# Optimization experiments

Measured on AMD Instinct MI355X. Metric: run time of the kernel, lower is better.

Reference implementation:

```python
import jax, jax.numpy as jnp
import numpy as np
import math

B, H, S, DK = 4, 16, 2048, 64

def setup_inputs() -> dict:
    key = jax.random.key(0)
    kq, kk, kv, km = jax.random.split(key, 4)
    q = jax.random.normal(kq, (B, H, S, DK), dtype=jnp.float32)
    k = jax.random.normal(kk, (B, H, S, DK), dtype=jnp.float32)
    v = jax.random.normal(kv, (B, H, S, DK), dtype=jnp.float32)
    mask = jax.random.randint(km, (B, 1, 1, S), 0, 2, dtype=jnp.int32)
    return {"q": q, "k": k, "v": v, "mask": mask}

def reference(q, k, v, mask):
    scale = 1.0 / math.sqrt(DK)
    # scores: [B, H, S, S]
    scores = jnp.einsum('bhqd,bhkd->bhqk', q, k) * scale
    scores = jnp.where(mask == 0, jnp.float32(-1e9), scores)
    attn = jax.nn.softmax(scores, axis=-1)
    out = jnp.einsum('bhqk,bhkd->bhqd', attn, v)
    return out
```

## Files before the change

### kernel.cpp

```cpp
#include <hip/hip_runtime.h>
#include <hip/hip_bf16.h>

#define S_LEN 2048
#define D_K   64
#define N_H   16
#define N_B   4
#define KVB   64
#define QPB   128
#define NQB   (S_LEN / QPB)
#define NBH   (N_B * N_H)
#define WS_NEED (2L * NBH * S_LEN * D_K * 2 + 4L * S_LEN * 4 + 16)

typedef __attribute__((ext_vector_type(8)))  short bf16x8;
typedef __attribute__((ext_vector_type(16))) float f32x16;
typedef unsigned int u32;
typedef __attribute__((ext_vector_type(4))) u32 u32x4;

__device__ inline short f2bfs(float x) {
    __hip_bfloat16 h = __float2bfloat16(x);
    return __builtin_bit_cast(short, h);
}

__device__ inline bf16x8 cvt8(const float* __restrict__ p) {
    float4 a = *(const float4*)p;
    float4 b = *(const float4*)(p + 4);
    bf16x8 f;
    f[0] = f2bfs(a.x); f[1] = f2bfs(a.y);
    f[2] = f2bfs(a.z); f[3] = f2bfs(a.w);
    f[4] = f2bfs(b.x); f[5] = f2bfs(b.y);
    f[6] = f2bfs(b.z); f[7] = f2bfs(b.w);
    return f;
}

__device__ inline bf16x8 cvt8s(const float* __restrict__ p, float s) {
    float4 a = *(const float4*)p;
    float4 b = *(const float4*)(p + 4);
    bf16x8 f;
    f[0] = f2bfs(a.x * s); f[1] = f2bfs(a.y * s);
    f[2] = f2bfs(a.z * s); f[3] = f2bfs(a.w * s);
    f[4] = f2bfs(b.x * s); f[5] = f2bfs(b.y * s);
    f[6] = f2bfs(b.z * s); f[7] = f2bfs(b.w * s);
    return f;
}

__device__ inline int vswz(int d) { return ((d & 7) ^ ((d >> 3) & 7)) << 4; }

__device__ inline void gld16(const void* g, void* l) {
    __builtin_amdgcn_global_load_lds(
        (const __attribute__((address_space(1))) void*)g,
        (__attribute__((address_space(3))) void*)l, 16, 0, 0);
}

__global__ __launch_bounds__(64)
void mask_scan(const int* __restrict__ mask, int* __restrict__ idx,
               int* __restrict__ cnt) {
    const int b = blockIdx.x, lane = threadIdx.x;
    const int* mb = mask + b * S_LEN;
    int base = 0;
    for (int j0 = 0; j0 < S_LEN; j0 += 64) {
        int mv = mb[j0 + lane];
        unsigned long long ball = __ballot(mv != 0);
        int pos = base + __popcll(ball & ((1ull << lane) - 1ull));
        if (mv) idx[b * S_LEN + pos] = j0 + lane;
        base += __popcll(ball);
    }
    if (lane == 0) cnt[b] = base;
}

__global__ __launch_bounds__(256)
void gather_cvt(const float* __restrict__ k, const float* __restrict__ v,
                const int* __restrict__ idx, const int* __restrict__ cnt,
                short* __restrict__ kc, short* __restrict__ vt) {
    const int bid = blockIdx.x, bh = bid >> 5, i0 = (bid & 31) * 64;
    const int b = bh >> 4;
    const int m = cnt[b];
    if (i0 >= ((m + 63) & ~63)) return;
    const int t = threadIdx.x;
    const int r = t >> 2, c0 = (t & 3) * 16;
    const int i = i0 + r;

    __shared__ __align__(16) short tile_[64][72];
    bf16x8 fv0, fv1, fk0, fk1;
    if (i < m) {
        const int src = idx[b * S_LEN + i];
        const float* kp = k + ((long)bh * S_LEN + src) * D_K + c0;
        const float* vp = v + ((long)bh * S_LEN + src) * D_K + c0;
        fk0 = cvt8(kp); fk1 = cvt8(kp + 8);
        fv0 = cvt8(vp); fv1 = cvt8(vp + 8);
    } else {
#pragma unroll
        for (int j = 0; j < 8; ++j) { fk0[j] = 0; fk1[j] = 0; fv0[j] = 0; fv1[j] = 0; }
    }
    short* kdst = kc + ((long)bh * S_LEN + i) * D_K + c0;
    *(bf16x8*)kdst       = fk0;
    *(bf16x8*)(kdst + 8) = fk1;
    *(bf16x8*)&tile_[r][c0]     = fv0;
    *(bf16x8*)&tile_[r][c0 + 8] = fv1;
    __syncthreads();
    const int dd = t >> 2, k0 = (t & 3) * 16;
    bf16x8 h0, h1;
#pragma unroll
    for (int j = 0; j < 8; ++j) {
        h0[j] = tile_[k0 + j][dd];
        h1[j] = tile_[k0 + 8 + j][dd];
    }
    short* dst = vt + ((long)bh * D_K + dd) * S_LEN + i0 + k0;
    *(bf16x8*)dst       = h0;
    *(bf16x8*)(dst + 8) = h1;
}

__global__ __launch_bounds__(256)
void attn_fwd(const float* __restrict__ q, const short* __restrict__ kbf,
              const short* __restrict__ vtb, const int* __restrict__ cnt,
              float* __restrict__ out) {
    const int id      = blockIdx.x;
    const int logical = (id & 7) * 128 + (id >> 3);
    const int bh      = logical >> 4;
    const int qblk    = logical & 15;
    const int b       = bh >> 4;
    const int t       = threadIdx.x;
    const int lane    = t & 63;
    const int wq      = t >> 6;
    const int hb      = lane >> 5;
    const int ql      = lane & 31;

    const int m   = cnt[b];
    const int NTr = (m + 63) >> 6;

    __shared__ __align__(16) short kbuf[2][KVB * D_K];
    __shared__ __align__(16) short vbuf[2][D_K * KVB];

    const float scale2 = 0.125f * 1.44269504f;
    const long  baseq  = (long)bh * S_LEN * D_K;
    const int   qrow0  = qblk * QPB + wq * 32;

    bf16x8 qf[4];
    {
        const float* qp = q + baseq + (long)(qrow0 + ql) * D_K + hb * 8;
#pragma unroll
        for (int kd = 0; kd < 4; ++kd) qf[kd] = cvt8s(qp + kd * 16, scale2);
    }

    const int lrow = lane >> 3, lchk = lane & 7;
    const int rA = wq * 16 + lrow;
    const int rB = rA + 8;
    const short* ksA = kbf + baseq + (long)rA * D_K + ((lchk ^ (rA & 7)) * 8);
    const short* ksB = kbf + baseq + (long)rB * D_K + ((lchk ^ (rB & 7)) * 8);
    const short* vsA = vtb + ((long)bh * D_K + rA) * S_LEN + ((lchk ^ ((rA & 7) ^ ((rA >> 3) & 7))) * 8);
    const short* vsB = vtb + ((long)bh * D_K + rB) * S_LEN + ((lchk ^ ((rB & 7) ^ ((rB >> 3) & 7))) * 8);

    auto STAGE_K = [&](int sel) {
        char* kdst = (char*)&kbuf[sel][0];
        gld16(ksA, kdst + (wq * 16) * 128);
        gld16(ksB, kdst + (wq * 16 + 8) * 128);
        ksA += KVB * D_K; ksB += KVB * D_K;
    };
    auto STAGE_V = [&](int sel) {
        char* vdst = (char*)&vbuf[sel][0];
        gld16(vsA, vdst + (wq * 16) * 128);
        gld16(vsB, vdst + (wq * 16 + 8) * 128);
        vsA += KVB; vsB += KVB;
    };

    f32x16 o0, o1;
#pragma unroll
    for (int r = 0; r < 16; ++r) { o0[r] = 0.f; o1[r] = 0.f; }
    float lrun = 0.f;

    f32x16 st0, st1;

    auto QK = [&](int kv0, int sel, bool lastt) {
        const char* kbp = (const char*)&kbuf[sel][0];
#pragma unroll
        for (int kb32 = 0; kb32 < 2; ++kb32) {
            f32x16 acc;
            if (!lastt) {
#pragma unroll
                for (int r = 0; r < 16; ++r) acc[r] = 0.f;
            } else {
                int keyb = kv0 + kb32 * 32 + 4 * hb;
#pragma unroll
                for (int r = 0; r < 16; ++r) {
                    int key = keyb + (r & 3) + 8 * (r >> 2);
                    acc[r] = (key < m) ? 0.f : -1e9f;
                }
            }
            int krow = kb32 * 32 + ql;
            int rb = krow * 128, sz = (krow & 7) << 4;
            __builtin_amdgcn_s_setprio(1);
#pragma unroll
            for (int kd = 0; kd < 4; ++kd) {
                bf16x8 kf = *(const bf16x8*)(kbp + ((rb + (kd * 16 + hb * 8) * 2) ^ sz));
                acc = __builtin_amdgcn_mfma_f32_32x32x16_bf16(kf, qf[kd], acc, 0, 0, 0);
            }
            __builtin_amdgcn_s_setprio(0);
            if (kb32 == 0) st0 = acc; else st1 = acc;
        }
    };

    STAGE_K(0);
    STAGE_V(0);
    if (NTr > 1) STAGE_K(1);
    __syncthreads();
    QK(0, 0, NTr == 1);
    __syncthreads();

    for (int tt = 0; tt < NTr; ++tt) {
        if (tt + 2 < NTr) STAGE_K(tt & 1);
        if (tt + 1 < NTr) STAGE_V((tt + 1) & 1);

        u32 w[2][8];
        float rs0 = 0.f, rs1 = 0.f;
#pragma unroll
        for (int mm = 0; mm < 8; ++mm) {
            float p0 = __builtin_amdgcn_exp2f(st0[2 * mm]);
            float p1 = __builtin_amdgcn_exp2f(st0[2 * mm + 1]);
            rs0 += p0; rs1 += p1;
            u32 r;
            asm("v_cvt_pk_bf16_f32 %0, %1, %2" : "=v"(r) : "v"(p0), "v"(p1));
            w[0][mm] = r;
        }
#pragma unroll
        for (int mm = 0; mm < 8; ++mm) {
            float p0 = __builtin_amdgcn_exp2f(st1[2 * mm]);
            float p1 = __builtin_amdgcn_exp2f(st1[2 * mm + 1]);
            rs0 += p0; rs1 += p1;
            u32 r;
            asm("v_cvt_pk_bf16_f32 %0, %1, %2" : "=v"(r) : "v"(p0), "v"(p1));
            w[1][mm] = r;
        }
        float rs = rs0 + rs1;
        rs += __shfl_xor(rs, 32, 64);
        lrun += rs;

        if (tt + 1 < NTr) QK((tt + 1) * KVB, (tt + 1) & 1, tt + 2 == NTr);

        const char* vbp = (const char*)&vbuf[tt & 1][0];
#pragma unroll
        for (int kbi = 0; kbi < 4; ++kbi) {
            int c = kbi >> 1, a2 = (kbi & 1) * 4;
            u32 x0 = w[c][a2 + 0], y0 = w[c][a2 + 2];
            u32 x1 = w[c][a2 + 1], y1 = w[c][a2 + 3];
            asm("v_permlane32_swap_b32 %0, %1" : "+v"(x0), "+v"(y0));
            asm("v_permlane32_swap_b32 %0, %1" : "+v"(x1), "+v"(y1));
            u32x4 av = {x0, x1, y0, y1};
            bf16x8 pa = __builtin_bit_cast(bf16x8, av);
            __builtin_amdgcn_s_setprio(1);
#pragma unroll
            for (int dn = 0; dn < 2; ++dn) {
                int d = dn * 32 + ql;
                bf16x8 vf = *(const bf16x8*)(vbp +
                              ((d * 128 + (kbi * 16 + hb * 8) * 2) ^ vswz(d)));
                if (dn == 0)
                    o0 = __builtin_amdgcn_mfma_f32_32x32x16_bf16(pa, vf, o0, 0, 0, 0);
                else
                    o1 = __builtin_amdgcn_mfma_f32_32x32x16_bf16(pa, vf, o1, 0, 0, 0);
            }
            __builtin_amdgcn_s_setprio(0);
        }

        __syncthreads();
    }

    float rl = 1.0f / lrun;
#pragma unroll
    for (int r = 0; r < 16; ++r) {
        int   cr  = (r & 3) + 8 * (r >> 2) + 4 * hb;
        float rlr = __shfl(rl, cr, 64);
        long  rowb = baseq + (long)(qrow0 + cr) * D_K;
        out[rowb + ql]      = o0[r] * rlr;
        out[rowb + 32 + ql] = o1[r] * rlr;
    }
}

__global__ __launch_bounds__(256)
void attn_fwd_legacy(const float* __restrict__ q, const float* __restrict__ k,
                     const float* __restrict__ v, const int* __restrict__ mask,
                     float* __restrict__ out) {
    const int id      = blockIdx.x;
    const int logical = (id & 7) * 128 + (id >> 3);
    const int bh      = logical >> 4;
    const int qblk    = logical & 15;
    const int b       = bh >> 4;
    const int t       = threadIdx.x;
    const int lane    = t & 63;
    const int wq      = t >> 6;
    const int hb      = lane >> 5;
    const int ql      = lane & 31;

    __shared__ __align__(16) short kbuf[KVB * D_K];
    __shared__ __align__(16) short vtbuf[D_K * KVB];
    __shared__ float mbias[S_LEN];

    const float scale2 = 0.125f * 1.44269504f;
    const long  base   = (long)bh * S_LEN * D_K;
    const int   qrow0  = qblk * QPB + wq * 32;

    {
        const int* mb = mask + b * S_LEN;
        for (int i = t; i < S_LEN; i += 256)
            mbias[i] = mb[i] ? 0.f : -1.442695e9f;
    }

    bf16x8 qf[4];
    {
        const float* qp = q + base + (long)(qrow0 + ql) * D_K + hb * 8;
#pragma unroll
        for (int kd = 0; kd < 4; ++kd) qf[kd] = cvt8s(qp + kd * 16, 1.0f);
    }

    f32x16 o0, o1;
#pragma unroll
    for (int r = 0; r < 16; ++r) { o0[r] = 0.f; o1[r] = 0.f; }
    float mrun = -1e30f, lrun = 0.f;

    const int srow = t >> 3;
    const int scol = t & 7;
    float4 kr[2][2], vr[2][2];

    auto LOADT = [&](int kv0) {
#pragma unroll
        for (int u2 = 0; u2 < 2; ++u2) {
            int row = srow + u2 * 32;
            const float* kp = k + base + (long)(kv0 + row) * D_K + scol * 8;
            const float* vp = v + base + (long)(kv0 + row) * D_K + scol * 8;
            kr[u2][0] = *(const float4*)kp; kr[u2][1] = *(const float4*)(kp + 4);
            vr[u2][0] = *(const float4*)vp; vr[u2][1] = *(const float4*)(vp + 4);
        }
    };

    LOADT(0);

    for (int tt = 0; tt < S_LEN / KVB; ++tt) {
        const int kv0 = tt * KVB;
        __syncthreads();
#pragma unroll
        for (int u2 = 0; u2 < 2; ++u2) {
            int row = srow + u2 * 32;
            bf16x8 fk, fv;
#pragma unroll
            for (int j = 0; j < 4; ++j) {
                fk[j]     = f2bfs(((const float*)&kr[u2][0])[j]);
                fk[j + 4] = f2bfs(((const float*)&kr[u2][1])[j]);
                fv[j]     = f2bfs(((const float*)&vr[u2][0])[j]);
                fv[j + 4] = f2bfs(((const float*)&vr[u2][1])[j]);
            }
            int kbyte = (row * 128 + scol * 16) ^ ((row & 7) << 4);
            *(bf16x8*)((char*)kbuf + kbyte) = fk;
#pragma unroll
            for (int j = 0; j < 8; ++j) {
                int d = scol * 8 + j;
                *(short*)((char*)vtbuf + ((d * 128 + row * 2) ^ vswz(d))) = fv[j];
            }
        }
        if (tt + 1 < S_LEN / KVB) LOADT(kv0 + KVB);
        __syncthreads();

        f32x16 stl[2];
#pragma unroll
        for (int kb32 = 0; kb32 < 2; ++kb32) {
            f32x16 acc;
#pragma unroll
            for (int r = 0; r < 16; ++r) acc[r] = 0.f;
            int krow = kb32 * 32 + ql;
            int rb = krow * 128, sz = (krow & 7) << 4;
#pragma unroll
            for (int kd = 0; kd < 4; ++kd) {
                bf16x8 kf = *(const bf16x8*)((const char*)kbuf + ((rb + (kd * 16 + hb * 8) * 2) ^ sz));
                acc = __builtin_amdgcn_mfma_f32_32x32x16_bf16(kf, qf[kd], acc, 0, 0, 0);
            }
            stl[kb32] = acc;
        }
#pragma unroll
        for (int kb32 = 0; kb32 < 2; ++kb32)
#pragma unroll
            for (int r = 0; r < 16; ++r) {
                int key = kv0 + kb32 * 32 + (r & 3) + 8 * (r >> 2) + 4 * hb;
                stl[kb32][r] = fmaf(stl[kb32][r], scale2, mbias[key]);
            }

        float m8[8];
#pragma unroll
        for (int i = 0; i < 8; ++i)
            m8[i] = fmaxf(fmaxf(stl[0][i], stl[0][i + 8]),
                          fmaxf(stl[1][i], stl[1][i + 8]));
        float tmax = fmaxf(fmaxf(fmaxf(m8[0], m8[1]), fmaxf(m8[2], m8[3])),
                           fmaxf(fmaxf(m8[4], m8[5]), fmaxf(m8[6], m8[7])));
        tmax = fmaxf(tmax, __shfl_xor(tmax, 32, 64));

        if (__any(tmax > mrun + 10.0f)) {
            float mnew = fmaxf(mrun, tmax);
            float al   = __builtin_amdgcn_exp2f(mrun - mnew);
            mrun = mnew;
            lrun *= al;
#pragma unroll
            for (int r = 0; r < 16; ++r) {
                float ar = __shfl(al, (r & 3) + 8 * (r >> 2) + 4 * hb, 64);
                o0[r] *= ar; o1[r] *= ar;
            }
        }

        u32 w[2][8];
        float rs = 0.f;
#pragma unroll
        for (int kb32 = 0; kb32 < 2; ++kb32)
#pragma unroll
            for (int mm = 0; mm < 8; ++mm) {
                float p0 = __builtin_amdgcn_exp2f(stl[kb32][2 * mm]     - mrun);
                float p1 = __builtin_amdgcn_exp2f(stl[kb32][2 * mm + 1] - mrun);
                rs += p0 + p1;
                w[kb32][mm] = (u32)(unsigned short)f2bfs(p0) |
                              ((u32)(unsigned short)f2bfs(p1) << 16);
            }
        rs += __shfl_xor(rs, 32, 64);
        lrun += rs;

#pragma unroll
        for (int kbi = 0; kbi < 4; ++kbi) {
            int c = kbi >> 1, a2 = (kbi & 1) * 4;
            u32 x0 = w[c][a2 + 0], y0 = w[c][a2 + 2];
            u32 x1 = w[c][a2 + 1], y1 = w[c][a2 + 3];
            asm("v_permlane32_swap_b32 %0, %1" : "+v"(x0), "+v"(y0));
            asm("v_permlane32_swap_b32 %0, %1" : "+v"(x1), "+v"(y1));
            u32x4 av = {x0, x1, y0, y1};
            bf16x8 pa = __builtin_bit_cast(bf16x8, av);
#pragma unroll
            for (int dn = 0; dn < 2; ++dn) {
                int d = dn * 32 + ql;
                bf16x8 vf = *(const bf16x8*)((const char*)vtbuf +
                              ((d * 128 + (kbi * 16 + hb * 8) * 2) ^ vswz(d)));
                if (dn == 0)
                    o0 = __builtin_amdgcn_mfma_f32_32x32x16_bf16(pa, vf, o0, 0, 0, 0);
                else
                    o1 = __builtin_amdgcn_mfma_f32_32x32x16_bf16(pa, vf, o1, 0, 0, 0);
            }
        }
    }

    float rl = 1.0f / lrun;
#pragma unroll
    for (int r = 0; r < 16; ++r) {
        int   cr  = (r & 3) + 8 * (r >> 2) + 4 * hb;
        float rlr = __shfl(rl, cr, 64);
        long  rowb = base + (long)(qrow0 + cr) * D_K;
        out[rowb + ql]      = o0[r] * rlr;
        out[rowb + 32 + ql] = o1[r] * rlr;
    }
}

extern "C" void kernel_launch(void* const* d_in, const int* in_sizes, int n_in,
                              void* d_out, int out_size, void* d_ws, size_t ws_size,
                              hipStream_t stream) {
    const float* q    = (const float*)d_in[0];
    const float* k    = (const float*)d_in[1];
    const float* v    = (const float*)d_in[2];
    const int*   mask = (const int*)d_in[3];
    float*       out  = (float*)d_out;

    if (ws_size >= (size_t)WS_NEED) {
        short* kc  = (short*)d_ws;
        short* vt  = kc + (long)NBH * S_LEN * D_K;
        int*   idx = (int*)(vt + (long)NBH * S_LEN * D_K);
        int*   cnt = idx + 4 * S_LEN;
        mask_scan<<<dim3(N_B), 64, 0, stream>>>(mask, idx, cnt);
        gather_cvt<<<dim3(NBH * (S_LEN / 64)), 256, 0, stream>>>(k, v, idx, cnt, kc, vt);
        attn_fwd<<<dim3(NQB * NBH), 256, 0, stream>>>(q, kc, vt, cnt, out);
    } else {
        attn_fwd_legacy<<<dim3(NQB * NBH), 256, 0, stream>>>(q, k, v, mask, out);
    }
}
```

Baseline: 82.77 us.

## Triple-buffer K/V LDS staging with explicit vmcnt waits and single barrier

K and V tiles are now staged through three LDS buffers instead of two, so loads run one tile further ahead. The per-iteration __syncthreads pair is replaced by an explicit s_waitcnt vmcnt with a count that depends on how many tiles remain, plus a raw s_barrier. The QK step also interleaves the two 32-key MFMA chains so their LDS reads and MFMAs can overlap. The cost is 50% more LDS per block, which may lower occupancy, and the hand-written vmcnt counts must match the number of outstanding async loads exactly.

Result: no change. 83.94 us (+1.4%).

```diff
diff --git a/kernel.cpp b/kernel.cpp
--- a/kernel.cpp
+++ b/kernel.cpp
@@ -127,8 +127,8 @@
     const int m   = cnt[b];
     const int NTr = (m + 63) >> 6;
 
-    __shared__ __align__(16) short kbuf[2][KVB * D_K];
-    __shared__ __align__(16) short vbuf[2][D_K * KVB];
+    __shared__ __align__(16) short kbuf[3][KVB * D_K];
+    __shared__ __align__(16) short vbuf[3][D_K * KVB];
 
     const float scale2 = 0.125f * 1.44269504f;
     const long  baseq  = (long)bh * S_LEN * D_K;
@@ -149,17 +149,17 @@
     const short* vsA = vtb + ((long)bh * D_K + rA) * S_LEN + ((lchk ^ ((rA & 7) ^ ((rA >> 3) & 7))) * 8);
     const short* vsB = vtb + ((long)bh * D_K + rB) * S_LEN + ((lchk ^ ((rB & 7) ^ ((rB >> 3) & 7))) * 8);
 
-    auto STAGE_K = [&](int sel) {
-        char* kdst = (char*)&kbuf[sel][0];
-        gld16(ksA, kdst + (wq * 16) * 128);
-        gld16(ksB, kdst + (wq * 16 + 8) * 128);
-        ksA += KVB * D_K; ksB += KVB * D_K;
+    auto STAGE_K = [&](int i) {
+        char* kdst = (char*)kbuf + (i % 3) * (KVB * D_K * 2);
+        long off = (long)i * (KVB * D_K);
+        gld16(ksA + off, kdst + (wq * 16) * 128);
+        gld16(ksB + off, kdst + (wq * 16 + 8) * 128);
     };
-    auto STAGE_V = [&](int sel) {
-        char* vdst = (char*)&vbuf[sel][0];
-        gld16(vsA, vdst + (wq * 16) * 128);
-        gld16(vsB, vdst + (wq * 16 + 8) * 128);
-        vsA += KVB; vsB += KVB;
+    auto STAGE_V = [&](int i) {
+        char* vdst = (char*)vbuf + (i % 3) * (D_K * KVB * 2);
+        long off = (long)i * KVB;
+        gld16(vsA + off, vdst + (wq * 16) * 128);
+        gld16(vsB + off, vdst + (wq * 16 + 8) * 128);
     };
 
     f32x16 o0, o1;
@@ -170,44 +170,55 @@
     f32x16 st0, st1;
 
     auto QK = [&](int kv0, int sel, bool lastt) {
-        const char* kbp = (const char*)&kbuf[sel][0];
-#pragma unroll
-        for (int kb32 = 0; kb32 < 2; ++kb32) {
-            f32x16 acc;
-            if (!lastt) {
-#pragma unroll
-                for (int r = 0; r < 16; ++r) acc[r] = 0.f;
-            } else {
-                int keyb = kv0 + kb32 * 32 + 4 * hb;
-#pragma unroll
-                for (int r = 0; r < 16; ++r) {
-                    int key = keyb + (r & 3) + 8 * (r >> 2);
-                    acc[r] = (key < m) ? 0.f : -1e9f;
-                }
-            }
-            int krow = kb32 * 32 + ql;
-            int rb = krow * 128, sz = (krow & 7) << 4;
-            __builtin_amdgcn_s_setprio(1);
-#pragma unroll
-            for (int kd = 0; kd < 4; ++kd) {
-                bf16x8 kf = *(const bf16x8*)(kbp + ((rb + (kd * 16 + hb * 8) * 2) ^ sz));
-                acc = __builtin_amdgcn_mfma_f32_32x32x16_bf16(kf, qf[kd], acc, 0, 0, 0);
-            }
-            __builtin_amdgcn_s_setprio(0);
-            if (kb32 == 0) st0 = acc; else st1 = acc;
-        }
+        const char* kbp = (const char*)kbuf + sel * (KVB * D_K * 2);
+        f32x16 a0, a1;
+        if (!lastt) {
+#pragma unroll
+            for (int r = 0; r < 16; ++r) { a0[r] = 0.f; a1[r] = 0.f; }
+        } else {
+            int keyb = kv0 + 4 * hb;
+#pragma unroll
+            for (int r = 0; r < 16; ++r) {
+                int key = keyb + (r & 3) + 8 * (r >> 2);
+                a0[r] = (key < m)      ? 0.f : -1e9f;
+                a1[r] = (key + 32 < m) ? 0.f : -1e9f;
+            }
+        }
+        int rb0 = (ql) * 128,      sz0 = (ql & 7) << 4;
+        int rb1 = (32 + ql) * 128, sz1 = sz0;
+        __builtin_amdgcn_s_setprio(1);
+#pragma unroll
+        for (int kd = 0; kd < 4; ++kd) {
+            int co = (kd * 16 + hb * 8) * 2;
+            bf16x8 kf0 = *(const bf16x8*)(kbp + ((rb0 + co) ^ sz0));
+            bf16x8 kf1 = *(const bf16x8*)(kbp + ((rb1 + co) ^ sz1));
+            a0 = __builtin_amdgcn_mfma_f32_32x32x16_bf16(kf0, qf[kd], a0, 0, 0, 0);
+            a1 = __builtin_amdgcn_mfma_f32_32x32x16_bf16(kf1, qf[kd], a1, 0, 0, 0);
+        }
+        __builtin_amdgcn_s_setprio(0);
+        st0 = a0; st1 = a1;
     };
 
     STAGE_K(0);
+    if (NTr > 1) STAGE_K(1);
     STAGE_V(0);
-    if (NTr > 1) STAGE_K(1);
-    __syncthreads();
+    if (NTr > 2) STAGE_K(2);
+    if (NTr > 1) STAGE_V(1);
+    if (NTr >= 3)      asm volatile("s_waitcnt vmcnt(8)" ::: "memory");
+    else if (NTr == 2) asm volatile("s_waitcnt vmcnt(6)" ::: "memory");
+    else               asm volatile("s_waitcnt vmcnt(2)" ::: "memory");
+    __builtin_amdgcn_s_barrier();
     QK(0, 0, NTr == 1);
-    __syncthreads();
 
     for (int tt = 0; tt < NTr; ++tt) {
-        if (tt + 2 < NTr) STAGE_K(tt & 1);
-        if (tt + 1 < NTr) STAGE_V((tt + 1) & 1);
+        int rem = ((tt + 2 < NTr) ? 2 : 0) + ((tt + 1 < NTr) ? 2 : 0);
+        if (rem == 4)      asm volatile("s_waitcnt vmcnt(4)" ::: "memory");
+        else if (rem == 2) asm volatile("s_waitcnt vmcnt(2)" ::: "memory");
+        else               asm volatile("s_waitcnt vmcnt(0)" ::: "memory");
+        __builtin_amdgcn_s_barrier();
+
+        if (tt + 3 < NTr) STAGE_K(tt + 3);
+        if (tt + 2 < NTr) STAGE_V(tt + 2);
 
         u32 w[2][8];
         float rs0 = 0.f, rs1 = 0.f;
@@ -233,9 +244,9 @@
         rs += __shfl_xor(rs, 32, 64);
         lrun += rs;
 
-        if (tt + 1 < NTr) QK((tt + 1) * KVB, (tt + 1) & 1, tt + 2 == NTr);
-
-        const char* vbp = (const char*)&vbuf[tt & 1][0];
+        if (tt + 1 < NTr) QK((tt + 1) * KVB, (tt + 1) % 3, tt + 2 == NTr);
+
+        const char* vbp = (const char*)vbuf + (tt % 3) * (D_K * KVB * 2);
 #pragma unroll
         for (int kbi = 0; kbi < 4; ++kbi) {
             int c = kbi >> 1, a2 = (kbi & 1) * 4;
@@ -258,8 +269,6 @@
             }
             __builtin_amdgcn_s_setprio(0);
         }
-
-        __syncthreads();
     }
 
     float rl = 1.0f / lrun;
```

## Double query rows per block to 256 with 8 waves sharing each K/V tile

Applied to the files above, without the earlier changes.

Raises the query block from 128 to 256 rows, launching 512-thread blocks (8 waves) so every K/V tile staged in shared memory is reused by twice as many query rows, halving global K/V traffic per output. Each wave now issues one async global-to-LDS load per K and V tile instead of two, and QK is restructured to interleave two independent MFMA chains. Block count halves to 512, which may reduce occupancy or load balance across CUs. The legacy path keeps its 128-row tiling via explicit constants.

New measurement: 83.12 us. About the same (+0.4%).

```diff
diff --git a/kernel.cpp b/kernel.cpp
--- a/kernel.cpp
+++ b/kernel.cpp
@@ -6,7 +6,7 @@
 #define N_H   16
 #define N_B   4
 #define KVB   64
-#define QPB   128
+#define QPB   256
 #define NQB   (S_LEN / QPB)
 #define NBH   (N_B * N_H)
 #define WS_NEED (2L * NBH * S_LEN * D_K * 2 + 4L * S_LEN * 4 + 16)
@@ -109,14 +109,14 @@
     *(bf16x8*)(dst + 8) = h1;
 }
 
-__global__ __launch_bounds__(256)
+__global__ __launch_bounds__(512)
 void attn_fwd(const float* __restrict__ q, const short* __restrict__ kbf,
               const short* __restrict__ vtb, const int* __restrict__ cnt,
               float* __restrict__ out) {
     const int id      = blockIdx.x;
-    const int logical = (id & 7) * 128 + (id >> 3);
-    const int bh      = logical >> 4;
-    const int qblk    = logical & 15;
+    const int logical = (id & 7) * 64 + (id >> 3);
+    const int bh      = logical >> 3;
+    const int qblk    = logical & 7;
     const int b       = bh >> 4;
     const int t       = threadIdx.x;
     const int lane    = t & 63;
@@ -142,24 +142,18 @@
     }
 
     const int lrow = lane >> 3, lchk = lane & 7;
-    const int rA = wq * 16 + lrow;
-    const int rB = rA + 8;
+    const int rA = wq * 8 + lrow;
     const short* ksA = kbf + baseq + (long)rA * D_K + ((lchk ^ (rA & 7)) * 8);
-    const short* ksB = kbf + baseq + (long)rB * D_K + ((lchk ^ (rB & 7)) * 8);
-    const short* vsA = vtb + ((long)bh * D_K + rA) * S_LEN + ((lchk ^ ((rA & 7) ^ ((rA >> 3) & 7))) * 8);
-    const short* vsB = vtb + ((long)bh * D_K + rB) * S_LEN + ((lchk ^ ((rB & 7) ^ ((rB >> 3) & 7))) * 8);
+    const short* vsA = vtb + ((long)bh * D_K + rA) * S_LEN
+                       + ((lchk ^ ((rA & 7) ^ ((rA >> 3) & 7))) * 8);
 
     auto STAGE_K = [&](int sel) {
-        char* kdst = (char*)&kbuf[sel][0];
-        gld16(ksA, kdst + (wq * 16) * 128);
-        gld16(ksB, kdst + (wq * 16 + 8) * 128);
-        ksA += KVB * D_K; ksB += KVB * D_K;
+        gld16(ksA, (char*)&kbuf[sel][0] + (wq * 8) * 128);
+        ksA += KVB * D_K;
     };
     auto STAGE_V = [&](int sel) {
-        char* vdst = (char*)&vbuf[sel][0];
-        gld16(vsA, vdst + (wq * 16) * 128);
-        gld16(vsB, vdst + (wq * 16 + 8) * 128);
-        vsA += KVB; vsB += KVB;
+        gld16(vsA, (char*)&vbuf[sel][0] + (wq * 8) * 128);
+        vsA += KVB;
     };
 
     f32x16 o0, o1;
@@ -171,31 +165,32 @@
 
     auto QK = [&](int kv0, int sel, bool lastt) {
         const char* kbp = (const char*)&kbuf[sel][0];
-#pragma unroll
-        for (int kb32 = 0; kb32 < 2; ++kb32) {
-            f32x16 acc;
-            if (!lastt) {
-#pragma unroll
-                for (int r = 0; r < 16; ++r) acc[r] = 0.f;
-            } else {
-                int keyb = kv0 + kb32 * 32 + 4 * hb;
-#pragma unroll
-                for (int r = 0; r < 16; ++r) {
-                    int key = keyb + (r & 3) + 8 * (r >> 2);
-                    acc[r] = (key < m) ? 0.f : -1e9f;
-                }
-            }
-            int krow = kb32 * 32 + ql;
-            int rb = krow * 128, sz = (krow & 7) << 4;
-            __builtin_amdgcn_s_setprio(1);
-#pragma unroll
-            for (int kd = 0; kd < 4; ++kd) {
-                bf16x8 kf = *(const bf16x8*)(kbp + ((rb + (kd * 16 + hb * 8) * 2) ^ sz));
-                acc = __builtin_amdgcn_mfma_f32_32x32x16_bf16(kf, qf[kd], acc, 0, 0, 0);
-            }
-            __builtin_amdgcn_s_setprio(0);
-            if (kb32 == 0) st0 = acc; else st1 = acc;
-        }
+        f32x16 a0, a1;
+        if (!lastt) {
+#pragma unroll
+            for (int r = 0; r < 16; ++r) { a0[r] = 0.f; a1[r] = 0.f; }
+        } else {
+            int keyb = kv0 + 4 * hb;
+#pragma unroll
+            for (int r = 0; r < 16; ++r) {
+                int key = keyb + (r & 3) + 8 * (r >> 2);
+                a0[r] = (key < m)      ? 0.f : -1e9f;
+                a1[r] = (key + 32 < m) ? 0.f : -1e9f;
+            }
+        }
+        int rb0 = (ql) * 128,      sz0 = (ql & 7) << 4;
+        int rb1 = (32 + ql) * 128, sz1 = sz0;
+        __builtin_amdgcn_s_setprio(1);
+#pragma unroll
+        for (int kd = 0; kd < 4; ++kd) {
+            int co = (kd * 16 + hb * 8) * 2;
+            bf16x8 kf0 = *(const bf16x8*)(kbp + ((rb0 + co) ^ sz0));
+            bf16x8 kf1 = *(const bf16x8*)(kbp + ((rb1 + co) ^ sz1));
+            a0 = __builtin_amdgcn_mfma_f32_32x32x16_bf16(kf0, qf[kd], a0, 0, 0, 0);
+            a1 = __builtin_amdgcn_mfma_f32_32x32x16_bf16(kf1, qf[kd], a1, 0, 0, 0);
+        }
+        __builtin_amdgcn_s_setprio(0);
+        st0 = a0; st1 = a1;
     };
 
     STAGE_K(0);
@@ -294,7 +289,7 @@
 
     const float scale2 = 0.125f * 1.44269504f;
     const long  base   = (long)bh * S_LEN * D_K;
-    const int   qrow0  = qblk * QPB + wq * 32;
+    const int   qrow0  = qblk * 128 + wq * 32;
 
     {
         const int* mb = mask + b * S_LEN;
@@ -464,8 +459,8 @@
         int*   cnt = idx + 4 * S_LEN;
         mask_scan<<<dim3(N_B), 64, 0, stream>>>(mask, idx, cnt);
         gather_cvt<<<dim3(NBH * (S_LEN / 64)), 256, 0, stream>>>(k, v, idx, cnt, kc, vt);
-        attn_fwd<<<dim3(NQB * NBH), 256, 0, stream>>>(q, kc, vt, cnt, out);
+        attn_fwd<<<dim3(NQB * NBH), 512, 0, stream>>>(q, kc, vt, cnt, out);
     } else {
-        attn_fwd_legacy<<<dim3(NQB * NBH), 256, 0, stream>>>(q, k, v, mask, out);
-    }
-}
+        attn_fwd_legacy<<<dim3((S_LEN / 128) * NBH), 256, 0, stream>>>(q, k, v, mask, out);
+    }
+}
```
